# Kernel tuning notes

Hardware: AMD Instinct MI355X
Metric: run time of the kernel (lower is better)

Reference implementation:

```python
import jax, jax.numpy as jnp
import numpy as np

B, T, E, H, DH = 8, 1024, 1024, 16, 64

def setup_inputs() -> dict:
    key = jax.random.key(0)
    ks = jax.random.split(key, 5)
    x = jax.random.normal(ks[0], (B, T, E), dtype=jnp.float32)
    Wq = jax.random.normal(ks[1], (H, E, DH), dtype=jnp.float32) * (E ** -0.5)
    Wk = jax.random.normal(ks[2], (H, E, DH), dtype=jnp.float32) * (E ** -0.5)
    Wv = jax.random.normal(ks[3], (H, E, DH), dtype=jnp.float32) * (E ** -0.5)
    Wp = jax.random.normal(ks[4], (E, E), dtype=jnp.float32) * (E ** -0.5)
    bp = jnp.zeros((E,), dtype=jnp.float32)
    return {"x": x, "Wq": Wq, "Wk": Wk, "Wv": Wv, "Wp": Wp, "bp": bp}

def reference(x, Wq, Wk, Wv, Wp, bp):
    # per-head projections (bias-free), vectorized over heads
    q = jnp.einsum('bte,hed->bhtd', x, Wq)
    k = jnp.einsum('bte,hed->bhtd', x, Wk)
    v = jnp.einsum('bte,hed->bhtd', x, Wv)
    scale = DH ** -0.5
    att = jnp.einsum('bhtd,bhsd->bhts', q, k) * scale  # [B,H,T,T]
    causal = jnp.tril(jnp.ones((T, T), dtype=bool))
    att = jnp.where(causal, att, -jnp.inf)
    att = jax.nn.softmax(att, axis=-1)
    # dropout is identity in eval mode
    out = jnp.einsum('bhts,bhsd->bhtd', att, v)
    out = out.transpose(0, 2, 1, 3).reshape(B, T, E)  # concat heads in order
    # proj: torch Linear y = x @ W^T + b
    out = out @ Wp.T + bp
    return out
```

## Files before the change

kernel.cpp:

```cpp
#include <hip/hip_runtime.h>

#define Bsz 8
#define Tsz 1024
#define Esz 1024
#define Hsz 16
#define DHsz 64
#define NQKV 3072

typedef _Float16 f16x8 __attribute__((ext_vector_type(8)));
typedef _Float16 f16x4 __attribute__((ext_vector_type(4)));
typedef float f32x4 __attribute__((ext_vector_type(4)));
typedef unsigned short u16x8 __attribute__((ext_vector_type(8)));

__device__ __forceinline__ unsigned short f2h(float f) {
    union { _Float16 h; unsigned short u; } cv;
    cv.h = (_Float16)f;
    return cv.u;
}

__device__ __forceinline__ unsigned int pkh2(float a, float b) {
    typedef __fp16 h16x2 __attribute__((ext_vector_type(2)));
    union { h16x2 v; unsigned int u; } cv;
    cv.v = __builtin_amdgcn_cvt_pkrtz(a, b);
    return cv.u;
}

__device__ __forceinline__ void async16(const void* g, void* l) {
    __builtin_amdgcn_global_load_lds(
        (const __attribute__((address_space(1))) void*)g,
        (__attribute__((address_space(3))) void*)l, 16, 0, 0);
}

#define MFMA(a, b, c)   __builtin_amdgcn_mfma_f32_16x16x32_f16((a), (b), (c), 0, 0, 0)
#define MFMA16(a, b, c) __builtin_amdgcn_mfma_f32_16x16x16f16((a), (b), (c), 0, 0, 0)


__global__ void cast_f16_kernel(const float* __restrict__ in, unsigned short* __restrict__ outp) {
    int i = (blockIdx.x * 256 + threadIdx.x) * 4;
    float4 v = *(const float4*)(in + i);
    ushort4 o;
    o.x = f2h(v.x); o.y = f2h(v.y); o.z = f2h(v.z); o.w = f2h(v.w);
    *(ushort4*)(outp + i) = o;
}

__global__ __launch_bounds__(256) void pack_wqkv_kernel(
    const float* __restrict__ Wq, const float* __restrict__ Wk,
    const float* __restrict__ Wv, unsigned short* __restrict__ Bt) {
    __shared__ unsigned int tile[64 * 33];
    const int blk = blockIdx.x;
    const int et = blk & 15, h = (blk >> 4) & 15, which = blk >> 8;
    const int tid = threadIdx.x;
    const float* W = (which == 0) ? Wq : ((which == 1) ? Wk : Wv);
    const float* src = W + ((size_t)h * Esz + et * 64) * DHsz;
#pragma unroll
    for (int it = 0; it < 4; ++it) {
        int task = tid + it * 256;
        int er = task >> 4, ds = task & 15;
        float4 v = *(const float4*)(src + (size_t)er * DHsz + ds * 4);
        tile[er * 33 + ds * 2]     = (unsigned int)f2h(v.x) | ((unsigned int)f2h(v.y) << 16);
        tile[er * 33 + ds * 2 + 1] = (unsigned int)f2h(v.z) | ((unsigned int)f2h(v.w) << 16);
    }
    __syncthreads();
    unsigned short* dst = Bt + ((size_t)(which * 1024 + h * 64)) * Esz + et * 64;
#pragma unroll
    for (int it = 0; it < 2; ++it) {
        int task = tid + it * 256;
        int d = task & 63, es = task >> 6;
        int du = d >> 1, hi = d & 1;
        u16x8 v;
#pragma unroll
        for (int j = 0; j < 8; ++j) {
            unsigned int w = tile[(es * 8 + j) * 33 + du];
            v[j] = (unsigned short)(hi ? (w >> 16) : (w & 0xffffu));
        }
        *(u16x8*)(dst + (size_t)d * Esz + es * 8) = v;
    }
}

__global__ __launch_bounds__(256) void vtrans_kernel(const unsigned short* __restrict__ QKV,
                                                     unsigned short* __restrict__ VT) {
    __shared__ unsigned int tile[64 * 33];
    const int bh = blockIdx.x, tc = blockIdx.y;
    const int b = bh >> 4, h = bh & 15;
    const int tid = threadIdx.x;
    const unsigned short* src = QKV + ((size_t)(b * Tsz) + tc * 64) * NQKV + 2048 + h * 64;
#pragma unroll
    for (int it = 0; it < 2; ++it) {
        int task = tid + it * 256;
        int row = task >> 3, seg = task & 7;
        u16x8 v = *(const u16x8*)(src + (size_t)row * NQKV + seg * 8);
#pragma unroll
        for (int jj = 0; jj < 4; ++jj)
            tile[row * 33 + seg * 4 + jj] =
                (unsigned int)v[2 * jj] | ((unsigned int)v[2 * jj + 1] << 16);
    }
    __syncthreads();
    unsigned short* dst = VT + (size_t)bh * DHsz * Tsz + tc * 64;
#pragma unroll
    for (int it = 0; it < 2; ++it) {
        int task = tid + it * 256;
        int d = task & 63, tseg = task >> 6;
        int du = d >> 1, hi = d & 1;
        u16x8 v;
#pragma unroll
        for (int j = 0; j < 8; ++j) {
            unsigned int w = tile[(tseg * 8 + j) * 33 + du];
            v[j] = (unsigned short)(hi ? (w >> 16) : (w & 0xffffu));
        }
        *(u16x8*)(dst + (size_t)d * Tsz + tseg * 8) = v;
    }
}

template <int MODE>
__global__ __launch_bounds__(256, 4) void gemm_bt(
    const unsigned short* __restrict__ A,
    const unsigned short* __restrict__ Bt,
    int K, int N,
    unsigned short* __restrict__ c16,
    float* __restrict__ outp, const float* __restrict__ bias)
{
    __shared__ unsigned short smem[17408];
    unsigned short* sA = smem;
    unsigned short* sB = smem + 4096;
    const int tid = threadIdx.x;
    const int wid = tid >> 6, lane = tid & 63;
    const int quad = lane >> 4, l16 = lane & 15;
    const int col0 = blockIdx.x * 128;
    const int row0 = blockIdx.y * 128;
    const int wm = (wid >> 1) * 64, wn = (wid & 1) * 64;

    const f32x4 zero4 = {0.f, 0.f, 0.f, 0.f};
    f32x4 acc[4][4];
#pragma unroll
    for (int i = 0; i < 4; ++i)
#pragma unroll
        for (int j = 0; j < 4; ++j) acc[i][j] = zero4;

    const unsigned short* gA = A + (size_t)row0 * K;
    const unsigned short* gB = Bt + (size_t)col0 * K;
    const int c0 = wid * 2;
    const int srw = lane >> 2;
    const int ssg = (lane & 3) * 8;

    for (int k0 = 0; k0 < K; k0 += 32) {
#pragma unroll
        for (int cc = 0; cc < 2; ++cc) {
            int c = c0 + cc;
            async16(gA + (size_t)(c * 16 + srw) * K + k0 + ssg, (void*)(sA + c * 512 + lane * 8));
            async16(gB + (size_t)(c * 16 + srw) * K + k0 + ssg, (void*)(sB + c * 512 + lane * 8));
        }
        __syncthreads();

        f16x8 af[4], bfr[4];
#pragma unroll
        for (int i = 0; i < 4; ++i)
            af[i] = *(const f16x8*)(sA + (wm + i * 16 + l16) * 32 + quad * 8);
#pragma unroll
        for (int j = 0; j < 4; ++j)
            bfr[j] = *(const f16x8*)(sB + (wn + j * 16 + l16) * 32 + quad * 8);
#pragma unroll
        for (int i = 0; i < 4; ++i)
#pragma unroll
            for (int j = 0; j < 4; ++j)
                acc[i][j] = MFMA(af[i], bfr[j], acc[i][j]);
        __syncthreads();
    }

    if (MODE == 0) {
#pragma unroll
        for (int i = 0; i < 4; ++i)
#pragma unroll
            for (int r = 0; r < 4; ++r) {
                int rowL = wm + i * 16 + quad * 4 + r;
                unsigned short* tr = smem + rowL * 136 + wn + l16;
#pragma unroll
                for (int j = 0; j < 4; ++j)
                    tr[j * 16] = f2h(acc[i][j][r]);
            }
        __syncthreads();
        unsigned short* ob = c16 + (size_t)row0 * N + col0;
#pragma unroll
        for (int it = 0; it < 8; ++it) {
            int rowG = wid * 32 + it * 4 + quad;
            u16x8 v = *(const u16x8*)(smem + rowG * 136 + l16 * 8);
            *(u16x8*)(ob + (size_t)rowG * N + l16 * 8) = v;
        }
    } else {
        float* ft = (float*)smem;
#pragma unroll
        for (int p = 0; p < 2; ++p) {
            __syncthreads();
            if ((wid >> 1) == p) {
#pragma unroll
                for (int i = 0; i < 4; ++i)
#pragma unroll
                    for (int r = 0; r < 4; ++r) {
                        int rowL = i * 16 + quad * 4 + r;
                        float* tr = ft + rowL * 136 + wn + l16;
#pragma unroll
                        for (int j = 0; j < 4; ++j)
                            tr[j * 16] = acc[i][j][r] + bias[col0 + wn + j * 16 + l16];
                    }
            }
            __syncthreads();
#pragma unroll
            for (int it = 0; it < 8; ++it) {
                int task = tid + it * 256;
                int rowL = task >> 5, cs = task & 31;
                float4 v = *(const float4*)(ft + rowL * 136 + cs * 4);
                *(float4*)(outp + (size_t)(row0 + p * 64 + rowL) * N + col0 + cs * 4) = v;
            }
        }
    }
}

__global__ __launch_bounds__(512, 6) void attn_kernel(
    const unsigned short* __restrict__ QKV,
    const unsigned short* __restrict__ VTg,
    unsigned short* __restrict__ AO)
{
    const int bh = blockIdx.x;
    const int pair = blockIdx.y;
    const int b = bh >> 4, h = bh & 15;
    const int tid = threadIdx.x, wid = tid >> 6, lane = tid & 63;
    const int quad = lane >> 4, l16 = lane & 15;

    __shared__ unsigned short smem[16384];
#define SKb(bf) (smem + (bf) * 4096)
#define SVb(bf) (smem + 8192 + (bf) * 4096)

    const unsigned short* Qb = QKV + (size_t)(b * Tsz) * NQKV + h * 64;
    const unsigned short* Kb = QKV + (size_t)(b * Tsz) * NQKV + 1024 + h * 64;
    const unsigned short* VTb = VTg + (size_t)bh * DHsz * Tsz;

    const int srow = lane >> 3;
    const int sseg = lane & 7;
    const int slog = sseg ^ srow;
    const int r0 = wid * 8;
    const int xk = l16 & 7;

    const float C1 = 0.18033688f;
    const float C2 = -4.32808512f;
    const f32x4 zero4 = {0.f, 0.f, 0.f, 0.f};

    for (int half = 0; half < 2; ++half) {
        const int qt = (half == 0) ? (7 - pair) : pair;
        const int q0 = qt * 128;
        const int rowlo = q0 + wid * 16;
        const int qrow = rowlo + l16;
        const int nblk = (q0 >> 6) + 2;

        __syncthreads();
        async16(Kb + (size_t)(r0 + srow) * NQKV + slog * 8, (void*)(SKb(0) + r0 * 64 + lane * 8));
        async16(VTb + (size_t)(r0 + srow) * Tsz + slog * 8, (void*)(SVb(0) + r0 * 64 + lane * 8));

        f16x8 qf[2];
#pragma unroll
        for (int kk = 0; kk < 2; ++kk)
            qf[kk] = *(const f16x8*)(Qb + (size_t)qrow * NQKV + kk * 32 + quad * 8);

        f32x4 o[4];
        float lp = 0.f;
#pragma unroll
        for (int dt = 0; dt < 4; ++dt) o[dt] = zero4;

        for (int blk = 0; blk < nblk; ++blk) {
            const int s0 = blk * 64;
            const int cur = blk & 1;
            __builtin_amdgcn_s_barrier();
            if (blk + 1 < nblk) {
                const int sn = (blk + 1) * 64;
                async16(Kb + (size_t)(sn + r0 + srow) * NQKV + slog * 8,
                        (void*)(SKb(cur ^ 1) + r0 * 64 + lane * 8));
                async16(VTb + (size_t)(r0 + srow) * Tsz + sn + slog * 8,
                        (void*)(SVb(cur ^ 1) + r0 * 64 + lane * 8));
                __asm__ volatile("s_waitcnt vmcnt(2)" ::: "memory");
            } else {
                __asm__ volatile("s_waitcnt vmcnt(0)" ::: "memory");
            }
            __builtin_amdgcn_s_barrier();
            __asm__ volatile("" ::: "memory");

            if (s0 > rowlo + 15) continue;

            f32x4 scT[4];
#pragma unroll
            for (int ct = 0; ct < 4; ++ct) scT[ct] = zero4;
#pragma unroll
            for (int kk = 0; kk < 2; ++kk) {
#pragma unroll
                for (int ct = 0; ct < 4; ++ct) {
                    f16x8 kf = *(const f16x8*)(SKb(cur) + (ct * 16 + l16) * 64 +
                                               (((kk * 4 + quad) ^ xk) * 8));
                    scT[ct] = MFMA(kf, qf[kk], scT[ct]);
                }
            }

            f16x4 pk[4];
            const bool full = (s0 + 63 <= rowlo);
#pragma unroll
            for (int ct = 0; ct < 4; ++ct) {
                int sb = s0 + ct * 16 + quad * 4;
                float p[4];
#pragma unroll
                for (int r = 0; r < 4; ++r) {
                    float v = exp2f(fmaf(scT[ct][r], C1, C2));
                    if (!full) v = (sb + r > qrow) ? 0.f : v;
                    p[r] = v;
                    lp += v;
                }
                union { f16x4 v; unsigned int u[2]; } cv;
                cv.u[0] = pkh2(p[0], p[1]);
                cv.u[1] = pkh2(p[2], p[3]);
                pk[ct] = cv.v;
            }

#pragma unroll
            for (int ct = 0; ct < 4; ++ct) {
                const int sl = 2 * ct + (quad >> 1);
#pragma unroll
                for (int dt = 0; dt < 4; ++dt) {
                    f16x4 vf = *(const f16x4*)(SVb(cur) + (dt * 16 + l16) * 64 +
                                               ((sl ^ xk) * 8) + (quad & 1) * 4);
                    o[dt] = MFMA16(vf, pk[ct], o[dt]);
                }
            }
        }

        float s = lp;
        s += __shfl_xor(s, 16, 64);
        s += __shfl_xor(s, 32, 64);
        float inv = 1.0f / s;

        __syncthreads();
        unsigned short* otr = smem;
        const int orow = wid * 16 + l16;
#pragma unroll
        for (int dt = 0; dt < 4; ++dt) {
            *(unsigned int*)(otr + orow * 72 + dt * 16 + quad * 4) =
                pkh2(o[dt][0] * inv, o[dt][1] * inv);
            *(unsigned int*)(otr + orow * 72 + dt * 16 + quad * 4 + 2) =
                pkh2(o[dt][2] * inv, o[dt][3] * inv);
        }
        __syncthreads();
#pragma unroll
        for (int it = 0; it < 2; ++it) {
            int rr = wid * 16 + it * 8 + srow;
            u16x8 v = *(const u16x8*)(otr + rr * 72 + sseg * 8);
            *(u16x8*)(AO + (size_t)(b * Tsz + q0 + rr) * Esz + h * 64 + sseg * 8) = v;
        }
    }
#undef SKb
#undef SVb
}


extern "C" void kernel_launch(void* const* d_in, const int* in_sizes, int n_in,
                              void* d_out, int out_size, void* d_ws, size_t ws_size,
                              hipStream_t stream)
{
    const float* x  = (const float*)d_in[0];
    const float* Wq = (const float*)d_in[1];
    const float* Wk = (const float*)d_in[2];
    const float* Wv = (const float*)d_in[3];
    const float* Wp = (const float*)d_in[4];
    const float* bp = (const float*)d_in[5];
    float* out = (float*)d_out;

    char* ws = (char*)d_ws;
    unsigned short* xb   = (unsigned short*)(ws);
    unsigned short* wqkv = (unsigned short*)(ws + 16777216);
    unsigned short* wpb  = (unsigned short*)(ws + 23068672);
    unsigned short* qkv  = (unsigned short*)(ws + 25165824);
    unsigned short* ao   = (unsigned short*)(ws + 75497472);
    unsigned short* vtb  = xb;

    cast_f16_kernel<<<8192, 256, 0, stream>>>(x, xb);
    pack_wqkv_kernel<<<768, 256, 0, stream>>>(Wq, Wk, Wv, wqkv);
    cast_f16_kernel<<<1024, 256, 0, stream>>>(Wp, wpb);

    gemm_bt<0><<<dim3(24, 64), 256, 0, stream>>>(xb, wqkv, 1024, 3072,
                                                 qkv, nullptr, nullptr);

    vtrans_kernel<<<dim3(128, 16), 256, 0, stream>>>(qkv, vtb);

    attn_kernel<<<dim3(128, 4), 512, 0, stream>>>(qkv, vtb, ao);

    gemm_bt<1><<<dim3(8, 64), 256, 0, stream>>>(ao, wpb, 1024, 1024,
                                                nullptr, out, bp);
}
```

Measured before the change: 248.2 us.

## Double-buffer GEMM LDS tiles with async prefetch and XOR swizzle

Converts the GEMM main loop from single-buffered (load, sync, compute, sync) to double-buffered LDS. The next K-tile is prefetched asynchronously while the current one is consumed, using explicit vmcnt waits and barriers. It also XOR-swizzles the 8-element column segments in shared memory to reduce LDS bank conflicts on fragment reads. This uses the existing 17408-element shared array more fully and relies on hand-placed waitcnt ordering for correctness.

```diff
diff --git a/kernel.cpp b/kernel.cpp
--- a/kernel.cpp
+++ b/kernel.cpp
@@ -120,8 +120,8 @@
     float* __restrict__ outp, const float* __restrict__ bias)
 {
     __shared__ unsigned short smem[17408];
-    unsigned short* sA = smem;
-    unsigned short* sB = smem + 4096;
+#define SAb(bf) (smem + (bf) * 4096)
+#define SBb(bf) (smem + 8192 + (bf) * 4096)
     const int tid = threadIdx.x;
     const int wid = tid >> 6, lane = tid & 63;
     const int quad = lane >> 4, l16 = lane & 15;
@@ -140,31 +140,52 @@
     const unsigned short* gB = Bt + (size_t)col0 * K;
     const int c0 = wid * 2;
     const int srw = lane >> 2;
-    const int ssg = (lane & 3) * 8;
-
-    for (int k0 = 0; k0 < K; k0 += 32) {
-#pragma unroll
-        for (int cc = 0; cc < 2; ++cc) {
-            int c = c0 + cc;
-            async16(gA + (size_t)(c * 16 + srw) * K + k0 + ssg, (void*)(sA + c * 512 + lane * 8));
-            async16(gB + (size_t)(c * 16 + srw) * K + k0 + ssg, (void*)(sB + c * 512 + lane * 8));
-        }
-        __syncthreads();
+    const int slog = (lane & 3) ^ (srw & 3);
+    const int xs = l16 & 3;
+
+    const int KSTEPS = K >> 5;
+#pragma unroll
+    for (int cc = 0; cc < 2; ++cc) {
+        int c = c0 + cc;
+        async16(gA + (size_t)(c * 16 + srw) * K + slog * 8, (void*)(SAb(0) + c * 512 + lane * 8));
+        async16(gB + (size_t)(c * 16 + srw) * K + slog * 8, (void*)(SBb(0) + c * 512 + lane * 8));
+    }
+
+#pragma unroll 2
+    for (int ks = 0; ks < KSTEPS; ++ks) {
+        const int cur = ks & 1;
+        __builtin_amdgcn_s_barrier();
+        if (ks + 1 < KSTEPS) {
+            const int kn = (ks + 1) * 32;
+#pragma unroll
+            for (int cc = 0; cc < 2; ++cc) {
+                int c = c0 + cc;
+                async16(gA + (size_t)(c * 16 + srw) * K + kn + slog * 8,
+                        (void*)(SAb(cur ^ 1) + c * 512 + lane * 8));
+                async16(gB + (size_t)(c * 16 + srw) * K + kn + slog * 8,
+                        (void*)(SBb(cur ^ 1) + c * 512 + lane * 8));
+            }
+            __asm__ volatile("s_waitcnt vmcnt(4)" ::: "memory");
+        } else {
+            __asm__ volatile("s_waitcnt vmcnt(0)" ::: "memory");
+        }
+        __builtin_amdgcn_s_barrier();
+        __asm__ volatile("" ::: "memory");
 
         f16x8 af[4], bfr[4];
 #pragma unroll
         for (int i = 0; i < 4; ++i)
-            af[i] = *(const f16x8*)(sA + (wm + i * 16 + l16) * 32 + quad * 8);
+            af[i] = *(const f16x8*)(SAb(cur) + (wm + i * 16 + l16) * 32 + ((quad ^ xs) * 8));
 #pragma unroll
         for (int j = 0; j < 4; ++j)
-            bfr[j] = *(const f16x8*)(sB + (wn + j * 16 + l16) * 32 + quad * 8);
+            bfr[j] = *(const f16x8*)(SBb(cur) + (wn + j * 16 + l16) * 32 + ((quad ^ xs) * 8));
 #pragma unroll
         for (int i = 0; i < 4; ++i)
 #pragma unroll
             for (int j = 0; j < 4; ++j)
                 acc[i][j] = MFMA(af[i], bfr[j], acc[i][j]);
-        __syncthreads();
-    }
+    }
+    __syncthreads();
 
     if (MODE == 0) {
 #pragma unroll
@@ -212,6 +233,8 @@
             }
         }
     }
+#undef SAb
+#undef SBb
 }
 
 __global__ __launch_bounds__(512, 6) void attn_kernel(
```

New measurement: 244.3 us. No clear change (-1.6%).
